# Kernel optimization log

Hardware: AMD Instinct MI355X
Metric: run time of the kernel (lower is better)

Reference implementation:

```python
import jax, jax.numpy as jnp
import numpy as np

B_, L_, D_, N_ = 4, 4096, 64, 16
DT = 0.1
EPS = 1e-6


def _complex_log(x):
    # log|x| (clamped) + i*pi for negative entries, matching torch impl
    real = jnp.log(jnp.maximum(jnp.abs(x), EPS))
    imag = jnp.where(x < 0, jnp.float32(np.pi), jnp.float32(0.0))
    return jax.lax.complex(real, imag)


def _clogaddexp(a, b):
    # stable complex log(exp(a)+exp(b)) using max of real parts
    m = jnp.maximum(a.real, b.real)
    return jnp.log(jnp.exp(a - m) + jnp.exp(b - m)) + m


def _clogcumsumexp(x, axis):
    return jax.lax.associative_scan(_clogaddexp, x, axis=axis)


def setup_inputs() -> dict:
    key = jax.random.key(0)
    ks = jax.random.split(key, 6)
    x = jax.random.normal(ks[0], (B_, L_, D_), jnp.float32)
    s = 1.0 / np.sqrt(D_)
    Wb = jax.random.uniform(ks[1], (N_, D_), jnp.float32, -s, s)
    bb = jax.random.uniform(ks[2], (N_,), jnp.float32, -s, s)
    Wc = jax.random.uniform(ks[3], (N_, D_), jnp.float32, -s, s)
    bc = jax.random.uniform(ks[4], (N_,), jnp.float32, -s, s)
    Wd = jax.random.uniform(ks[5], (1, D_), jnp.float32, -s, s)
    bd = jnp.zeros((1,), jnp.float32)
    # S4D-Real init: A_n = -(n+1), repeated over input_dim rows -> (D, N)
    A = jnp.tile(-(jnp.arange(N_, dtype=jnp.float32) + 1.0)[None, :], (D_, 1))
    return {"x": x, "A": A, "Wb": Wb, "bb": bb, "Wc": Wc, "bc": bc,
            "Wd": Wd, "bd": bd}


def reference(x, A, Wb, bb, Wc, bc, Wd, bd):
    # projections: (b,l,n)
    Bm = x @ Wb.T + bb
    Cm = x @ Wc.T + bc
    # delta network: softplus(linear(x)) + dt, broadcast to input_dim
    delta = jax.nn.softplus(x @ Wd.T + bd) + DT            # (b,l,1)
    dt = jnp.broadcast_to(delta, x.shape)                  # (b,l,d)
    # discretize
    tmp = A * dt[..., None]                                # (b,l,d,n)
    A_bar = jnp.exp(tmp)
    delta_B = jnp.einsum('bld,bln->bldn', dt, Bm)
    B_bar = (A_bar - 1.0) * delta_B / (tmp + EPS)
    term2 = B_bar * x[..., None]                           # (b,l,d,n)
    # parallel scan via complex log-cumsum-exp trick
    log_a = _complex_log(A_bar)
    log_b = _complex_log(term2)
    a_star = jnp.cumsum(log_a, axis=1)                     # (b,l,d,n) complex
    t = _clogcumsumexp(log_b - a_star, axis=1)
    scan = jnp.exp(a_star + t).real                        # (b,l,d,n)
    return jnp.sum(scan * Cm[:, :, None, :], axis=-1)      # (b,l,d)
```

## Files before the change

kernel.cpp:

```cpp
#include <hip/hip_runtime.h>

#define B_ 4
#define L_ 4096
#define D_ 64
#define N_ 16
#define CHUNK 16
#define NCHUNK (L_ / CHUNK)
#define TOTCHUNK (B_ * NCHUNK)

constexpr float DT_  = 0.1f;
constexpr float EPS_ = 1e-6f;

__global__ __launch_bounds__(256) void proj_scan_kernel(
    const float* __restrict__ x,  const float* __restrict__ A,
    const float* __restrict__ Wb, const float* __restrict__ bb,
    const float* __restrict__ Wc, const float* __restrict__ bc,
    const float* __restrict__ Wd, const float* __restrict__ bd,
    float* __restrict__ S, float* __restrict__ Cdec,
    float* __restrict__ Wcor, float* __restrict__ out)
{
    const int gc    = blockIdx.x;
    const int batch = gc >> 8;
    const int c     = gc & (NCHUNK - 1);
    const int tid   = threadIdx.x;
    const int w     = tid >> 6;
    const int lane  = tid & 63;
    const int base0 = batch * L_ + c * CHUNK;

    __shared__ float xs[CHUNK * D_];
    __shared__ float ag[CHUNK * 32];
    __shared__ float cm[CHUNK * N_];
    __shared__ float wbuf[CHUNK * N_];
    __shared__ float pout[4 * CHUNK * D_];

    ((float4*)xs)[tid] = ((const float4*)(x + (size_t)base0 * D_))[tid];

    const int o  = lane & 31;
    const int h2 = lane >> 5;
    float wreg[32];
    const float* Wrow = (o < 16) ? (Wb + o * D_) : (Wc + (o - 16) * D_);
    const float4* w4p = (const float4*)(Wrow + h2 * 32);
    #pragma unroll
    for (int j = 0; j < 8; j++) {
        float4 w4 = w4p[j];
        wreg[4*j+0] = w4.x; wreg[4*j+1] = w4.y;
        wreg[4*j+2] = w4.z; wreg[4*j+3] = w4.w;
    }
    const float wd   = Wd[lane];
    const float bd0  = bd[0];
    const float An   = A[lane & 15];
    const float bias = (o < 16) ? bb[o] : bc[o - 16];

    __syncthreads();

    const int s0 = w * 4;
    float r[4];
    #pragma unroll
    for (int p = 0; p < 4; p++) r[p] = xs[(s0 + p) * D_ + lane] * wd;
    #pragma unroll
    for (int m = 32; m >= 1; m >>= 1) {
        #pragma unroll
        for (int p = 0; p < 4; p++) r[p] += __shfl_xor(r[p], m, 64);
    }
    float delta[4];
    #pragma unroll
    for (int p = 0; p < 4; p++) {
        float z = r[p] + bd0;
        delta[p] = fmaxf(z, 0.0f) + log1pf(expf(-fabsf(z))) + DT_;
    }

    #pragma unroll
    for (int p = 0; p < 4; p++) {
        const int s = s0 + p;
        float acc = 0.0f;
        const float4* xs4 = (const float4*)(xs + s * D_ + h2 * 32);
        #pragma unroll
        for (int j = 0; j < 8; j++) {
            float4 v = xs4[j];
            acc += v.x * wreg[4*j+0] + v.y * wreg[4*j+1]
                 + v.z * wreg[4*j+2] + v.w * wreg[4*j+3];
        }
        acc += __shfl_xor(acc, 32, 64);
        if (lane < 16) {
            float Bm  = acc + bias;
            float tmp = An * delta[p];
            float a   = expf(tmp);
            float g   = (a - 1.0f) * delta[p] * Bm / (tmp + EPS_);
            ag[s * 32 + lane]      = a;
            ag[s * 32 + 16 + lane] = g;
        } else if (lane < 32) {
            cm[s * 16 + (lane - 16)] = acc + bias;
        }
    }
    __syncthreads();

    const int n0 = w * 4;
    float h0 = 0.0f, h1 = 0.0f, h2v = 0.0f, h3 = 0.0f;
    #pragma unroll
    for (int s = 0; s < CHUNK; s++) {
        float  xd = xs[s * D_ + lane];
        float4 a4 = *(const float4*)(ag + s * 32 + n0);
        float4 g4 = *(const float4*)(ag + s * 32 + 16 + n0);
        float4 c4 = *(const float4*)(cm + s * 16 + n0);
        h0 = a4.x * h0 + g4.x * xd;  float acc = c4.x * h0;
        h1 = a4.y * h1 + g4.y * xd;  acc += c4.y * h1;
        h2v = a4.z * h2v + g4.z * xd; acc += c4.z * h2v;
        h3 = a4.w * h3 + g4.w * xd;  acc += c4.w * h3;
        pout[(w * CHUNK + s) * D_ + lane] = acc;
    }
    S[(size_t)(gc * N_ + n0 + 0) * D_ + lane] = h0;
    S[(size_t)(gc * N_ + n0 + 1) * D_ + lane] = h1;
    S[(size_t)(gc * N_ + n0 + 2) * D_ + lane] = h2v;
    S[(size_t)(gc * N_ + n0 + 3) * D_ + lane] = h3;

    if (tid < 16) {
        float cumn = 1.0f;
        #pragma unroll
        for (int s = 0; s < CHUNK; s++) {
            cumn *= ag[s * 32 + tid];
            wbuf[s * 16 + tid] = cm[s * 16 + tid] * cumn;
        }
        Cdec[gc * N_ + tid] = cumn;
    }
    __syncthreads();

    #pragma unroll
    for (int k = 0; k < 4; k++) {
        const int f = k * 256 + tid;
        float v = pout[f] + pout[CHUNK * D_ + f]
                + pout[2 * CHUNK * D_ + f] + pout[3 * CHUNK * D_ + f];
        out[(size_t)base0 * D_ + f] = v;
    }
    if (tid < 64)
        ((float4*)(Wcor + (size_t)base0 * 16))[tid] = ((const float4*)wbuf)[tid];
}

#define G_ 32
__global__ __launch_bounds__(64) void combine(
    float* __restrict__ S, const float* __restrict__ Cdec)
{
    const int b = blockIdx.x >> 4;
    const int n = blockIdx.x & 15;
    const int d = threadIdx.x;
    const int cb = b * NCHUNK;

    float*       baseS = S    + (size_t)(cb * N_ + n) * D_ + d;
    const float* baseA = Cdec + cb * N_ + n;

    float run = 0.0f;
    float sbuf[G_], abuf[G_];
    #pragma unroll
    for (int j = 0; j < G_; j++) {
        sbuf[j] = baseS[(size_t)j * (N_ * D_)];
        abuf[j] = baseA[j * N_];
    }
    for (int cc = 0; cc < NCHUNK; cc += G_) {
        const int cn = (cc + G_ < NCHUNK) ? (cc + G_) : cc;
        float t[G_], u[G_];
        #pragma unroll
        for (int j = 0; j < G_; j++) {
            t[j] = baseS[(size_t)(cn + j) * (N_ * D_)];
            u[j] = baseA[(cn + j) * N_];
        }
        #pragma unroll
        for (int j = 0; j < G_; j++) {
            baseS[(size_t)(cc + j) * (N_ * D_)] = run;
            run = abuf[j] * run + sbuf[j];
        }
        #pragma unroll
        for (int j = 0; j < G_; j++) { sbuf[j] = t[j]; abuf[j] = u[j]; }
    }
}

__global__ __launch_bounds__(256) void apply_kernel(
    const float* __restrict__ Wcor, const float* __restrict__ S,
    float* __restrict__ out)
{
    const int gc    = blockIdx.x;
    const int batch = gc >> 8;
    const int c     = gc & (NCHUNK - 1);
    const int tid   = threadIdx.x;
    const int w     = tid >> 6;
    const int lane  = tid & 63;
    const int base0 = batch * L_ + c * CHUNK;

    __shared__ float wl[CHUNK * N_];

    if (tid < 64)
        ((float4*)wl)[tid] = ((const float4*)(Wcor + (size_t)base0 * 16))[tid];

    float hi[N_];
    #pragma unroll
    for (int n = 0; n < N_; n++)
        hi[n] = S[(size_t)(gc * N_ + n) * D_ + lane];

    const int s0 = w * 4;
    float oreg[4];
    #pragma unroll
    for (int p = 0; p < 4; p++)
        oreg[p] = out[(size_t)(base0 + s0 + p) * D_ + lane];

    __syncthreads();

    #pragma unroll
    for (int p = 0; p < 4; p++) {
        const int s = s0 + p;
        const float4* crw = (const float4*)(wl + s * 16);
        float a = oreg[p];
        #pragma unroll
        for (int q = 0; q < 4; q++) {
            float4 w4 = crw[q];
            a += w4.x * hi[4*q+0] + w4.y * hi[4*q+1]
               + w4.z * hi[4*q+2] + w4.w * hi[4*q+3];
        }
        out[(size_t)(base0 + s) * D_ + lane] = a;
    }
}

extern "C" void kernel_launch(void* const* d_in, const int* in_sizes, int n_in,
                              void* d_out, int out_size, void* d_ws, size_t ws_size,
                              hipStream_t stream)
{
    const float* x  = (const float*)d_in[0];
    const float* A  = (const float*)d_in[1];
    const float* Wb = (const float*)d_in[2];
    const float* bb = (const float*)d_in[3];
    const float* Wc = (const float*)d_in[4];
    const float* bc = (const float*)d_in[5];
    const float* Wd = (const float*)d_in[6];
    const float* bd = (const float*)d_in[7];
    float* out = (float*)d_out;

    float* S    = (float*)d_ws;
    float* Cdec = S    + (size_t)TOTCHUNK * N_ * D_;
    float* Wcor = Cdec + (size_t)TOTCHUNK * N_;

    proj_scan_kernel<<<TOTCHUNK, 256, 0, stream>>>(x, A, Wb, bb, Wc, bc, Wd, bd,
                                                   S, Cdec, Wcor, out);
    combine<<<B_ * N_, 64, 0, stream>>>(S, Cdec);
    apply_kernel<<<TOTCHUNK, 256, 0, stream>>>(Wcor, S, out);
}
```

Baseline: 100.3 us.

## Fuse three kernels into one cooperative kernel with matrix-form intra-chunk scan

Replaces the three launches (chunk scan, cross-chunk combine, apply) with a single cooperative kernel that separates the phases with grid.sync. The intra-chunk recurrence becomes a closed form: cumulative delta sums give decay exponentials, a 16x16 lower-triangular mixing matrix produces the local outputs, and chunk end states come from weighted sums. The combine step runs on 64 blocks with a smaller prefetch group, and the original three-kernel path is kept as a fallback if the cooperative launch fails. This removes launch gaps and intermediate round trips through global memory, at the cost of two grid-wide barriers during which most blocks sit idle, more exp calls, and a device attribute query on every launch.

```diff
diff --git a/kernel.cpp b/kernel.cpp
--- a/kernel.cpp
+++ b/kernel.cpp
@@ -1,4 +1,7 @@
 #include <hip/hip_runtime.h>
+#include <hip/hip_cooperative_groups.h>
+
+namespace cg = cooperative_groups;
 
 #define B_ 4
 #define L_ 4096
@@ -10,6 +13,188 @@
 
 constexpr float DT_  = 0.1f;
 constexpr float EPS_ = 1e-6f;
+
+__global__ __launch_bounds__(256, 4) void fused_kernel(
+    const float* __restrict__ x,  const float* __restrict__ A,
+    const float* __restrict__ Wb, const float* __restrict__ bb,
+    const float* __restrict__ Wc, const float* __restrict__ bc,
+    const float* __restrict__ Wd, const float* __restrict__ bd,
+    float* __restrict__ S, float* __restrict__ Cdec,
+    float* __restrict__ out)
+{
+    cg::grid_group grid = cg::this_grid();
+    const int gc    = blockIdx.x;
+    const int batch = gc >> 8;
+    const int c     = gc & (NCHUNK - 1);
+    const int tid   = threadIdx.x;
+    const int w     = tid >> 6;
+    const int lane  = tid & 63;
+    const int base0 = batch * L_ + c * CHUNK;
+
+    __shared__ float xs[CHUNK * D_];
+    __shared__ float AnS[N_];
+    __shared__ float dl[CHUNK];
+    __shared__ float DsS[CHUNK];
+    __shared__ float bmS[CHUNK * N_];
+    __shared__ float cmS[CHUNK * N_];
+    __shared__ float gT[N_ * CHUNK];
+    __shared__ float uS[CHUNK * N_];
+    __shared__ float wnjS[CHUNK * N_];
+    __shared__ float MS[CHUNK * CHUNK];
+    __shared__ float his[N_ * D_];
+
+    ((float4*)xs)[tid] = ((const float4*)(x + (size_t)base0 * D_))[tid];
+    if (tid < N_) AnS[tid] = A[tid];
+
+    const int o  = lane & 31;
+    const int h2 = lane >> 5;
+    float wreg[32];
+    const float* Wrow = (o < 16) ? (Wb + o * D_) : (Wc + (o - 16) * D_);
+    const float4* w4p = (const float4*)(Wrow + h2 * 32);
+    #pragma unroll
+    for (int j = 0; j < 8; j++) {
+        float4 w4 = w4p[j];
+        wreg[4*j+0] = w4.x; wreg[4*j+1] = w4.y;
+        wreg[4*j+2] = w4.z; wreg[4*j+3] = w4.w;
+    }
+    const float wd   = Wd[lane];
+    const float bd0  = bd[0];
+    const float bias = (o < 16) ? bb[o] : bc[o - 16];
+
+    __syncthreads();
+
+    const int s0 = w * 4;
+    float r[4];
+    #pragma unroll
+    for (int p = 0; p < 4; p++) r[p] = xs[(s0 + p) * D_ + lane] * wd;
+    #pragma unroll
+    for (int m = 32; m >= 1; m >>= 1) {
+        #pragma unroll
+        for (int p = 0; p < 4; p++) r[p] += __shfl_xor(r[p], m, 64);
+    }
+    #pragma unroll
+    for (int p = 0; p < 4; p++) {
+        float z = r[p] + bd0;
+        float dlt = fmaxf(z, 0.0f) + log1pf(expf(-fabsf(z))) + DT_;
+        if (lane == 0) dl[s0 + p] = dlt;
+    }
+
+    #pragma unroll
+    for (int p = 0; p < 4; p++) {
+        const int s = s0 + p;
+        float acc = 0.0f;
+        const float4* xs4 = (const float4*)(xs + s * D_ + h2 * 32);
+        #pragma unroll
+        for (int j = 0; j < 8; j++) {
+            float4 v = xs4[j];
+            acc += v.x * wreg[4*j+0] + v.y * wreg[4*j+1]
+                 + v.z * wreg[4*j+2] + v.w * wreg[4*j+3];
+        }
+        acc += __shfl_xor(acc, 32, 64);
+        if (lane < 16)      bmS[s * 16 + lane]        = acc + bias;
+        else if (lane < 32) cmS[s * 16 + (lane - 16)] = acc + bias;
+    }
+    __syncthreads();
+
+    {
+        const int s = tid >> 4, n = tid & 15;
+        float ds = 0.0f, dsF = 0.0f;
+        #pragma unroll
+        for (int k = 0; k < CHUNK; k++) {
+            float v = dl[k];
+            dsF += v;
+            if (k <= s) ds += v;
+        }
+        const float An  = AnS[n];
+        const float dls = dl[s];
+        const float tmp = An * dls;
+        const float a   = expf(tmp);
+        const float g   = (a - 1.0f) * dls * bmS[tid] / (tmp + EPS_);
+        gT[n * 16 + s]  = g;
+        uS[tid]         = cmS[tid] * expf(An * ds);
+        wnjS[tid]       = expf(An * (dsF - ds)) * g;
+        if (n == 0) DsS[s] = ds;
+        if (tid < 16) Cdec[gc * N_ + tid] = expf(AnS[tid] * dsF);
+    }
+    __syncthreads();
+
+    {
+        const int s = tid >> 4, j = tid & 15;
+        float m = 0.0f;
+        if (j <= s) {
+            const float dd = DsS[s] - DsS[j];
+            #pragma unroll
+            for (int n = 0; n < N_; n++)
+                m += cmS[s * 16 + n] * expf(AnS[n] * dd) * gT[n * 16 + j];
+        }
+        MS[tid] = m;
+    }
+    __syncthreads();
+
+    const int d = lane;
+    float oreg[4];
+    #pragma unroll
+    for (int k = 0; k < 4; k++) {
+        const int sn = w * 4 + k;
+        float acc = 0.0f, acc2 = 0.0f;
+        #pragma unroll
+        for (int j = 0; j < CHUNK; j++) {
+            const float xv = xs[j * 64 + d];
+            acc  += MS[sn * 16 + j]   * xv;
+            acc2 += wnjS[j * 16 + sn] * xv;
+        }
+        oreg[k] = acc;
+        S[(size_t)(gc * N_ + sn) * D_ + d] = acc2;
+    }
+
+    grid.sync();
+
+#define G2 16
+    if (blockIdx.x < B_ * N_ && tid < 64) {
+        const int b = blockIdx.x >> 4;
+        const int n = blockIdx.x & 15;
+        float*       baseS = S    + (size_t)((b * NCHUNK) * N_ + n) * D_ + lane;
+        const float* baseA = Cdec + (b * NCHUNK) * N_ + n;
+
+        float run = 0.0f;
+        float sbuf[G2], abuf[G2];
+        #pragma unroll
+        for (int j = 0; j < G2; j++) {
+            sbuf[j] = baseS[(size_t)j * (N_ * D_)];
+            abuf[j] = baseA[j * N_];
+        }
+        for (int cc = 0; cc < NCHUNK; cc += G2) {
+            const int cn = (cc + G2 < NCHUNK) ? (cc + G2) : cc;
+            float t[G2], u[G2];
+            #pragma unroll
+            for (int j = 0; j < G2; j++) {
+                t[j] = baseS[(size_t)(cn + j) * (N_ * D_)];
+                u[j] = baseA[(cn + j) * N_];
+            }
+            #pragma unroll
+            for (int j = 0; j < G2; j++) {
+                baseS[(size_t)(cc + j) * (N_ * D_)] = run;
+                run = abuf[j] * run + sbuf[j];
+            }
+            #pragma unroll
+            for (int j = 0; j < G2; j++) { sbuf[j] = t[j]; abuf[j] = u[j]; }
+        }
+    }
+
+    grid.sync();
+
+    ((float4*)his)[tid] = ((const float4*)(S + (size_t)gc * N_ * D_))[tid];
+    __syncthreads();
+    #pragma unroll
+    for (int k = 0; k < 4; k++) {
+        const int s = w * 4 + k;
+        float corr = 0.0f;
+        #pragma unroll
+        for (int n = 0; n < N_; n++)
+            corr += uS[s * 16 + n] * his[n * 64 + d];
+        out[(size_t)(base0 + s) * D_ + d] = oreg[k] + corr;
+    }
+}
 
 __global__ __launch_bounds__(256) void proj_scan_kernel(
     const float* __restrict__ x,  const float* __restrict__ A,
@@ -229,14 +414,32 @@
     const float* bc = (const float*)d_in[5];
     const float* Wd = (const float*)d_in[6];
     const float* bd = (const float*)d_in[7];
-    float* out = (float*)d_out;
+    float* outp = (float*)d_out;
 
     float* S    = (float*)d_ws;
     float* Cdec = S    + (size_t)TOTCHUNK * N_ * D_;
     float* Wcor = Cdec + (size_t)TOTCHUNK * N_;
 
-    proj_scan_kernel<<<TOTCHUNK, 256, 0, stream>>>(x, A, Wb, bb, Wc, bc, Wd, bd,
-                                                   S, Cdec, Wcor, out);
-    combine<<<B_ * N_, 64, 0, stream>>>(S, Cdec);
-    apply_kernel<<<TOTCHUNK, 256, 0, stream>>>(Wcor, S, out);
+    int dev = 0, coop = 0;
+    hipGetDevice(&dev);
+    hipDeviceGetAttribute(&coop, hipDeviceAttributeCooperativeLaunch, dev);
+
+    bool launched = false;
+    if (coop) {
+        void* args[] = { (void*)&x, (void*)&A, (void*)&Wb, (void*)&bb,
+                         (void*)&Wc, (void*)&bc, (void*)&Wd, (void*)&bd,
+                         (void*)&S, (void*)&Cdec, (void*)&outp };
+        hipError_t err = hipLaunchCooperativeKernel(
+            (const void*)fused_kernel, dim3(TOTCHUNK), dim3(256),
+            args, 0, stream);
+        launched = (err == hipSuccess);
+    }
+
+    if (!launched) {
+        proj_scan_kernel<<<TOTCHUNK, 256, 0, stream>>>(x, A, Wb, bb, Wc, bc,
+                                                       Wd, bd, S, Cdec, Wcor,
+                                                       outp);
+        combine<<<B_ * N_, 64, 0, stream>>>(S, Cdec);
+        apply_kernel<<<TOTCHUNK, 256, 0, stream>>>(Wcor, S, outp);
+    }
 }
```

Result: slower. 378.9 us (+277.9%).

## Replace per-chunk sequential recurrence with matrix-form intra-chunk SSM computation

Applied to the files above, without the earlier changes.

Within each chunk, the serial 16-step state recurrence is replaced by a matrix form. A per-chunk 16x16 decay-weighted kernel M is built from cumulative delta sums, so the chunk output becomes M times x. The chunk-end states and the carry weights come from closed-form exponentials of the cumulative deltas rather than running products. The apply kernel also stages the state tile in shared memory. This removes the serial dependency chain and the partial-sum buffers, but adds many more expf evaluations (16 per M entry) and changes rounding behaviour.

```diff
diff --git a/kernel.cpp b/kernel.cpp
--- a/kernel.cpp
+++ b/kernel.cpp
@@ -28,12 +28,18 @@
     const int base0 = batch * L_ + c * CHUNK;
 
     __shared__ float xs[CHUNK * D_];
-    __shared__ float ag[CHUNK * 32];
-    __shared__ float cm[CHUNK * N_];
-    __shared__ float wbuf[CHUNK * N_];
-    __shared__ float pout[4 * CHUNK * D_];
+    __shared__ float AnS[N_];
+    __shared__ float dl[CHUNK];
+    __shared__ float DsS[CHUNK];
+    __shared__ float bmS[CHUNK * N_];
+    __shared__ float cmS[CHUNK * N_];
+    __shared__ float gT[N_ * CHUNK];
+    __shared__ float uS[CHUNK * N_];
+    __shared__ float wnjS[CHUNK * N_];
+    __shared__ float MS[CHUNK * CHUNK];
 
     ((float4*)xs)[tid] = ((const float4*)(x + (size_t)base0 * D_))[tid];
+    if (tid < N_) AnS[tid] = A[tid];
 
     const int o  = lane & 31;
     const int h2 = lane >> 5;
@@ -48,7 +54,6 @@
     }
     const float wd   = Wd[lane];
     const float bd0  = bd[0];
-    const float An   = A[lane & 15];
     const float bias = (o < 16) ? bb[o] : bc[o - 16];
 
     __syncthreads();
@@ -62,11 +67,11 @@
         #pragma unroll
         for (int p = 0; p < 4; p++) r[p] += __shfl_xor(r[p], m, 64);
     }
-    float delta[4];
     #pragma unroll
     for (int p = 0; p < 4; p++) {
         float z = r[p] + bd0;
-        delta[p] = fmaxf(z, 0.0f) + log1pf(expf(-fabsf(z))) + DT_;
+        float dlt = fmaxf(z, 0.0f) + log1pf(expf(-fabsf(z))) + DT_;
+        if (lane == 0) dl[s0 + p] = dlt;
     }
 
     #pragma unroll
@@ -81,58 +86,63 @@
                  + v.z * wreg[4*j+2] + v.w * wreg[4*j+3];
         }
         acc += __shfl_xor(acc, 32, 64);
-        if (lane < 16) {
-            float Bm  = acc + bias;
-            float tmp = An * delta[p];
-            float a   = expf(tmp);
-            float g   = (a - 1.0f) * delta[p] * Bm / (tmp + EPS_);
-            ag[s * 32 + lane]      = a;
-            ag[s * 32 + 16 + lane] = g;
-        } else if (lane < 32) {
-            cm[s * 16 + (lane - 16)] = acc + bias;
-        }
-    }
-    __syncthreads();
-
-    const int n0 = w * 4;
-    float h0 = 0.0f, h1 = 0.0f, h2v = 0.0f, h3 = 0.0f;
-    #pragma unroll
-    for (int s = 0; s < CHUNK; s++) {
-        float  xd = xs[s * D_ + lane];
-        float4 a4 = *(const float4*)(ag + s * 32 + n0);
-        float4 g4 = *(const float4*)(ag + s * 32 + 16 + n0);
-        float4 c4 = *(const float4*)(cm + s * 16 + n0);
-        h0 = a4.x * h0 + g4.x * xd;  float acc = c4.x * h0;
-        h1 = a4.y * h1 + g4.y * xd;  acc += c4.y * h1;
-        h2v = a4.z * h2v + g4.z * xd; acc += c4.z * h2v;
-        h3 = a4.w * h3 + g4.w * xd;  acc += c4.w * h3;
-        pout[(w * CHUNK + s) * D_ + lane] = acc;
-    }
-    S[(size_t)(gc * N_ + n0 + 0) * D_ + lane] = h0;
-    S[(size_t)(gc * N_ + n0 + 1) * D_ + lane] = h1;
-    S[(size_t)(gc * N_ + n0 + 2) * D_ + lane] = h2v;
-    S[(size_t)(gc * N_ + n0 + 3) * D_ + lane] = h3;
-
-    if (tid < 16) {
-        float cumn = 1.0f;
-        #pragma unroll
-        for (int s = 0; s < CHUNK; s++) {
-            cumn *= ag[s * 32 + tid];
-            wbuf[s * 16 + tid] = cm[s * 16 + tid] * cumn;
-        }
-        Cdec[gc * N_ + tid] = cumn;
-    }
-    __syncthreads();
-
+        if (lane < 16)      bmS[s * 16 + lane]        = acc + bias;
+        else if (lane < 32) cmS[s * 16 + (lane - 16)] = acc + bias;
+    }
+    __syncthreads();
+
+    {
+        const int s = tid >> 4, n = tid & 15;
+        float ds = 0.0f, dsF = 0.0f;
+        #pragma unroll
+        for (int k = 0; k < CHUNK; k++) {
+            float v = dl[k];
+            dsF += v;
+            if (k <= s) ds += v;
+        }
+        const float An  = AnS[n];
+        const float dls = dl[s];
+        const float tmp = An * dls;
+        const float a   = expf(tmp);
+        const float g   = (a - 1.0f) * dls * bmS[tid] / (tmp + EPS_);
+        gT[n * 16 + s]  = g;
+        uS[tid]         = cmS[tid] * expf(An * ds);
+        wnjS[tid]       = expf(An * (dsF - ds)) * g;
+        if (n == 0) DsS[s] = ds;
+        if (tid < 16) Cdec[gc * N_ + tid] = expf(AnS[tid] * dsF);
+    }
+    __syncthreads();
+
+    {
+        const int s = tid >> 4, j = tid & 15;
+        float m = 0.0f;
+        if (j <= s) {
+            const float dd = DsS[s] - DsS[j];
+            #pragma unroll
+            for (int n = 0; n < N_; n++)
+                m += cmS[s * 16 + n] * expf(AnS[n] * dd) * gT[n * 16 + j];
+        }
+        MS[tid] = m;
+    }
+    __syncthreads();
+
+    const int d = lane;
     #pragma unroll
     for (int k = 0; k < 4; k++) {
-        const int f = k * 256 + tid;
-        float v = pout[f] + pout[CHUNK * D_ + f]
-                + pout[2 * CHUNK * D_ + f] + pout[3 * CHUNK * D_ + f];
-        out[(size_t)base0 * D_ + f] = v;
-    }
+        const int sn = w * 4 + k;
+        float acc = 0.0f, acc2 = 0.0f;
+        #pragma unroll
+        for (int j = 0; j < CHUNK; j++) {
+            const float xv = xs[j * 64 + d];
+            acc  += MS[sn * 16 + j]   * xv;
+            acc2 += wnjS[j * 16 + sn] * xv;
+        }
+        out[(size_t)(base0 + sn) * D_ + d] = acc;
+        S[(size_t)(gc * N_ + sn) * D_ + d] = acc2;
+    }
+
     if (tid < 64)
-        ((float4*)(Wcor + (size_t)base0 * 16))[tid] = ((const float4*)wbuf)[tid];
+        ((float4*)(Wcor + (size_t)base0 * 16))[tid] = ((const float4*)uS)[tid];
 }
 
 #define G_ 32
@@ -185,15 +195,13 @@
     const int base0 = batch * L_ + c * CHUNK;
 
     __shared__ float wl[CHUNK * N_];
+    __shared__ float his[N_ * D_];
+
+    ((float4*)his)[tid] = ((const float4*)(S + (size_t)gc * N_ * D_))[tid];
 
     if (tid < 64)
         ((float4*)wl)[tid] = ((const float4*)(Wcor + (size_t)base0 * 16))[tid];
 
-    float hi[N_];
-    #pragma unroll
-    for (int n = 0; n < N_; n++)
-        hi[n] = S[(size_t)(gc * N_ + n) * D_ + lane];
-
     const int s0 = w * 4;
     float oreg[4];
     #pragma unroll
@@ -205,14 +213,10 @@
     #pragma unroll
     for (int p = 0; p < 4; p++) {
         const int s = s0 + p;
-        const float4* crw = (const float4*)(wl + s * 16);
         float a = oreg[p];
         #pragma unroll
-        for (int q = 0; q < 4; q++) {
-            float4 w4 = crw[q];
-            a += w4.x * hi[4*q+0] + w4.y * hi[4*q+1]
-               + w4.z * hi[4*q+2] + w4.w * hi[4*q+3];
-        }
+        for (int n = 0; n < N_; n++)
+            a += wl[s * 16 + n] * his[n * 64 + lane];
         out[(size_t)(base0 + s) * D_ + lane] = a;
     }
 }
```

Result: no change. 100.7 us (+0.5%).
